# Kernel optimization log

Hardware: AMD Instinct MI355X
Metric: run time of the kernel (lower is better)

## Reference

```python
import jax, jax.numpy as jnp
import numpy as np

N_HEADS = 16

def setup_inputs() -> dict:
    key = jax.random.key(0)
    k1, k2, k3 = jax.random.split(key, 3)
    d = 1024
    x = jax.random.normal(k1, (4, 2048, d), dtype=jnp.float32)
    w_qkv = jax.random.normal(k2, (d, 3 * d), dtype=jnp.float32) * (1.0 / np.sqrt(d))
    w_proj = jax.random.normal(k3, (d, d), dtype=jnp.float32) * (1.0 / np.sqrt(d))
    return {"x": x, "w_qkv": w_qkv, "w_proj": w_proj}

def reference(x, w_qkv, w_proj):
    b, s, c = x.shape
    h = N_HEADS
    hd = c // h
    qkv = x @ w_qkv  # [b, s, 3c]
    q, k, v = jnp.split(qkv, 3, axis=-1)
    # [b, h, s, hd]
    q = q.reshape(b, s, h, hd).transpose(0, 2, 1, 3)
    k = k.reshape(b, s, h, hd).transpose(0, 2, 1, 3)
    v = v.reshape(b, s, h, hd).transpose(0, 2, 1, 3)
    scores = jnp.einsum('bhqd,bhkd->bhqk', q, k) / jnp.sqrt(jnp.float32(hd))
    causal = jnp.tril(jnp.ones((s, s), dtype=bool))
    scores = jnp.where(causal[None, None], scores, jnp.float32(-jnp.inf))
    attn = jax.nn.softmax(scores, axis=-1)
    out = jnp.einsum('bhqk,bhkd->bhqd', attn, v)
    out = out.transpose(0, 2, 1, 3).reshape(b, s, c)
    return out @ w_proj
```

## Files before the change

kernel.cpp:

```cpp
#include <hip/hip_runtime.h>
#include <hip/hip_bf16.h>

typedef unsigned short u16;
typedef __attribute__((ext_vector_type(8))) short short8;
typedef __attribute__((ext_vector_type(4))) float f32x4;
typedef __attribute__((ext_vector_type(16))) float f32x16;

__device__ inline u16 f2bf(float f) {
  unsigned u = __float_as_uint(f);
  u += 0x7fffu + ((u >> 16) & 1u);
  return (u16)(u >> 16);
}

__global__ __launch_bounds__(256) void cast_kernel(const float* __restrict__ in,
                                                   u16* __restrict__ out, int n4) {
  int i = blockIdx.x * 256 + threadIdx.x;
  if (i >= n4) return;
  float4 v = ((const float4*)in)[i];
  ushort4 o;
  o.x = f2bf(v.x); o.y = f2bf(v.y); o.z = f2bf(v.z); o.w = f2bf(v.w);
  ((ushort4*)out)[i] = o;
}

__global__ __launch_bounds__(256) void tcast_kernel(const float* __restrict__ in,
                                                    u16* __restrict__ out, int K, int N) {
  __shared__ float tile[32][33];
  int bx = blockIdx.x * 32;
  int by = blockIdx.y * 32;
  int tx = threadIdx.x & 31, ty = threadIdx.x >> 5;
#pragma unroll
  for (int i = 0; i < 4; i++) {
    int r = ty + i * 8;
    tile[r][tx] = in[(size_t)(by + r) * N + bx + tx];
  }
  __syncthreads();
#pragma unroll
  for (int i = 0; i < 4; i++) {
    int r = ty + i * 8;
    out[(size_t)(bx + r) * K + by + tx] = f2bf(tile[tx][r]);
  }
}

__global__ __launch_bounds__(256) void pack_kv(const u16* __restrict__ kbuf,
                                               const u16* __restrict__ vbuf,
                                               u16* __restrict__ kpack,
                                               u16* __restrict__ vpack) {
  __shared__ __align__(16) u16 ktile[64 * 72];
  __shared__ __align__(16) u16 vtile[64 * 72];
  int t = threadIdx.x;
  int kt = blockIdx.x, h = blockIdx.y, b = blockIdx.z;
  int bh = b * 16 + h;
  size_t rb = (size_t)(b * 2048 + kt * 64);
#pragma unroll
  for (int i = 0; i < 2; i++) {
    int idx = i * 256 + t; int r = idx >> 3, c8 = (idx & 7) * 8;
    *(uint4*)&ktile[r * 72 + c8] = *(const uint4*)(kbuf + (rb + r) * 1024 + h * 64 + c8);
    *(uint4*)&vtile[r * 72 + c8] = *(const uint4*)(vbuf + (rb + r) * 1024 + h * 64 + c8);
  }
  __syncthreads();
  u16* kd = kpack + ((size_t)bh * 32 + kt) * 4096;
  u16* vd = vpack + ((size_t)bh * 32 + kt) * 4096;
#pragma unroll
  for (int i = 0; i < 2; i++) {
    int idx = i * 256 + t;
    int j = idx >> 6, lane = idx & 63, l31 = lane & 31, hi5 = lane >> 5;
    *(uint4*)(kd + j * 512 + lane * 8) =
        *(const uint4*)&ktile[((j >> 2) * 32 + l31) * 72 + (j & 3) * 16 + hi5 * 8];
    union { u16 s[8]; uint4 u; } pv;
#pragma unroll
    for (int e = 0; e < 8; e++)
      pv.s[e] = vtile[((j & 3) * 16 + hi5 * 8 + e) * 72 + (j >> 2) * 32 + l31];
    *(uint4*)(vd + j * 512 + lane * 8) = pv.u;
  }
}

#define GEMM_BODY(KSTR)                                                                       \
  __shared__ __align__(16) u16 As[128 * 32];                                                  \
  __shared__ __align__(16) u16 Bs[128 * 32];                                                  \
  int t = threadIdx.x;                                                                        \
  int wave = t >> 6, lane = t & 63, l15 = lane & 15, quad = lane >> 4;                        \
  int bn = blockIdx.x * 128, bm = blockIdx.y * 128;                                           \
  int wm = (wave >> 1) * 64, wn = (wave & 1) * 64;                                            \
  f32x4 acc[4][4];                                                                            \
  for (int i = 0; i < 4; i++)                                                                 \
    for (int j = 0; j < 4; j++) acc[i][j] = (f32x4)0.0f;                                      \
  int srow = wave * 16 + (lane >> 2);                                                         \
  int scol = (lane & 3) * 8;                                                                  \
  const u16* ga0 = A + (size_t)(bm + srow) * KSTR + scol;                                     \
  const u16* ga1 = A + (size_t)(bm + 64 + srow) * KSTR + scol;                                \
  const u16* gb0 = Bt + (size_t)(bn + srow) * KSTR + scol;                                    \
  const u16* gb1 = Bt + (size_t)(bn + 64 + srow) * KSTR + scol;                               \
  u16* lA0 = As + wave * 512;                                                                 \
  u16* lA1 = As + 2048 + wave * 512;                                                          \
  u16* lB0 = Bs + wave * 512;                                                                 \
  u16* lB1 = Bs + 2048 + wave * 512;                                                          \
  for (int k0 = 0; k0 < KSTR; k0 += 32) {                                                     \
    __syncthreads();                                                                          \
    __builtin_amdgcn_global_load_lds((const __attribute__((address_space(1))) unsigned*)(ga0 + k0), \
                                     (__attribute__((address_space(3))) unsigned*)lA0, 16, 0, 0);   \
    __builtin_amdgcn_global_load_lds((const __attribute__((address_space(1))) unsigned*)(ga1 + k0), \
                                     (__attribute__((address_space(3))) unsigned*)lA1, 16, 0, 0);   \
    __builtin_amdgcn_global_load_lds((const __attribute__((address_space(1))) unsigned*)(gb0 + k0), \
                                     (__attribute__((address_space(3))) unsigned*)lB0, 16, 0, 0);   \
    __builtin_amdgcn_global_load_lds((const __attribute__((address_space(1))) unsigned*)(gb1 + k0), \
                                     (__attribute__((address_space(3))) unsigned*)lB1, 16, 0, 0);   \
    __syncthreads();                                                                          \
    short8 a[4], b[4];                                                                        \
    for (int mt = 0; mt < 4; mt++)                                                            \
      a[mt] = *(const short8*)(&As[(wm + mt * 16 + l15) * 32 + quad * 8]);                    \
    for (int nt = 0; nt < 4; nt++)                                                            \
      b[nt] = *(const short8*)(&Bs[(wn + nt * 16 + l15) * 32 + quad * 8]);                    \
    for (int mt = 0; mt < 4; mt++)                                                            \
      for (int nt = 0; nt < 4; nt++)                                                          \
        acc[mt][nt] = __builtin_amdgcn_mfma_f32_16x16x32_bf16(a[mt], b[nt], acc[mt][nt], 0, 0, 0); \
  }

__global__ __launch_bounds__(256) void gemm_qkv(const u16* __restrict__ A,
                                                const u16* __restrict__ Bt,
                                                u16* __restrict__ qb,
                                                u16* __restrict__ kb,
                                                u16* __restrict__ vb) {
  GEMM_BODY(1024)
  u16* dst = (bn < 1024) ? qb : (bn < 2048) ? kb : vb;
  float scl = (bn < 1024) ? 0.18033688011112f : 1.0f;
  int bnl = bn & 1023;
#pragma unroll
  for (int mt = 0; mt < 4; mt++)
#pragma unroll
    for (int nt = 0; nt < 4; nt++)
#pragma unroll
      for (int r = 0; r < 4; r++) {
        int row = bm + wm + mt * 16 + quad * 4 + r;
        int col = bnl + wn + nt * 16 + l15;
        dst[(size_t)row * 1024 + col] = f2bf(acc[mt][nt][r] * scl);
      }
}

__global__ __launch_bounds__(256) void gemm_proj(const u16* __restrict__ A,
                                                 const u16* __restrict__ Bt,
                                                 float* __restrict__ Co) {
  GEMM_BODY(1024)
#pragma unroll
  for (int mt = 0; mt < 4; mt++)
#pragma unroll
    for (int nt = 0; nt < 4; nt++)
#pragma unroll
      for (int r = 0; r < 4; r++) {
        int row = bm + wm + mt * 16 + quad * 4 + r;
        int col = bn + wn + nt * 16 + l15;
        Co[(size_t)row * 1024 + col] = acc[mt][nt][r];
      }
}

__global__ __launch_bounds__(256, 2) void attn_kernel(const u16* __restrict__ qbuf,
                                                      const u16* __restrict__ kpack,
                                                      const u16* __restrict__ vpack,
                                                      u16* __restrict__ ctx) {
  int t = threadIdx.x;
  int wave = t >> 6, lane = t & 63, l31 = lane & 31, hi = lane >> 5;
  int bh = blockIdx.x;
  int s = (int)blockIdx.y * 4 + wave;
  int b = bh >> 4, h = bh & 15;
  int rowbase = b * 2048;
  int hi4 = hi * 4;

  const u16* kp = kpack + (size_t)bh * (32 * 4096) + lane * 8;
  const u16* vp = vpack + (size_t)bh * (32 * 4096) + lane * 8;

#pragma unroll
  for (int ph = 0; ph < 2; ph++) {
    int strip = ph ? 63 - s : s;
    int q0 = strip * 32;
    int q_lane = q0 + l31;

    const u16* qp = qbuf + (size_t)(rowbase + q_lane) * 1024 + h * 64 + hi * 8;
    short8 qf[4];
#pragma unroll
    for (int ks = 0; ks < 4; ks++) qf[ks] = *(const short8*)(qp + ks * 16);

    float l_run = 0.0f;
    f32x16 o[2];
    o[0] = (f32x16)0.0f; o[1] = (f32x16)0.0f;
    int ktmax = (q0 + 31) >> 6;

    for (int kt = 0; kt <= ktmax; kt++) {
      const u16* kb = kp + kt * 4096;
      const u16* vb = vp + kt * 4096;

      short8 ka[8], vv[8];
#pragma unroll
      for (int j = 0; j < 8; j++) {
        ka[j] = *(const short8*)(kb + j * 512);
        vv[j] = *(const short8*)(vb + j * 512);
      }

      f32x16 st0 = (f32x16)0.0f, st1 = (f32x16)0.0f;
#pragma unroll
      for (int ks = 0; ks < 4; ks++) {
        st0 = __builtin_amdgcn_mfma_f32_32x32x16_bf16(ka[ks], qf[ks], st0, 0, 0, 0);
        st1 = __builtin_amdgcn_mfma_f32_32x32x16_bf16(ka[4 + ks], qf[ks], st1, 0, 0, 0);
      }

      unsigned pk[2][8];
      if (kt == ktmax) {
#pragma unroll
        for (int ii = 0; ii < 8; ii++) {
          int key = kt * 64 + ((2 * ii) & 3) + 8 * ((2 * ii) >> 2) + hi4;
          float p00 = (key     <= q_lane) ? __builtin_amdgcn_exp2f(st0[2 * ii])     : 0.0f;
          float p01 = (key + 1 <= q_lane) ? __builtin_amdgcn_exp2f(st0[2 * ii + 1]) : 0.0f;
          float p10 = (key + 32 <= q_lane) ? __builtin_amdgcn_exp2f(st1[2 * ii])     : 0.0f;
          float p11 = (key + 33 <= q_lane) ? __builtin_amdgcn_exp2f(st1[2 * ii + 1]) : 0.0f;
          l_run += p00 + p01 + p10 + p11;
          pk[0][ii] = ((__float_as_uint(p00) + 0x8000u) >> 16) |
                      ((__float_as_uint(p01) + 0x8000u) & 0xffff0000u);
          pk[1][ii] = ((__float_as_uint(p10) + 0x8000u) >> 16) |
                      ((__float_as_uint(p11) + 0x8000u) & 0xffff0000u);
        }
      } else {
#pragma unroll
        for (int ii = 0; ii < 8; ii++) {
          float p00 = __builtin_amdgcn_exp2f(st0[2 * ii]);
          float p01 = __builtin_amdgcn_exp2f(st0[2 * ii + 1]);
          float p10 = __builtin_amdgcn_exp2f(st1[2 * ii]);
          float p11 = __builtin_amdgcn_exp2f(st1[2 * ii + 1]);
          l_run += p00 + p01 + p10 + p11;
          pk[0][ii] = ((__float_as_uint(p00) + 0x8000u) >> 16) |
                      ((__float_as_uint(p01) + 0x8000u) & 0xffff0000u);
          pk[1][ii] = ((__float_as_uint(p10) + 0x8000u) >> 16) |
                      ((__float_as_uint(p11) + 0x8000u) & 0xffff0000u);
        }
      }

      short8 pf[4];
#pragma unroll
      for (int ks2 = 0; ks2 < 4; ks2++) {
        int km = ks2 >> 1, h4 = (ks2 & 1) * 4;
        unsigned A0 = pk[km][h4 + 0], A1 = pk[km][h4 + 1];
        unsigned B0 = pk[km][h4 + 2], B1 = pk[km][h4 + 3];
        unsigned tA0 = (unsigned)__shfl_xor((int)A0, 32);
        unsigned tA1 = (unsigned)__shfl_xor((int)A1, 32);
        unsigned tB0 = (unsigned)__shfl_xor((int)B0, 32);
        unsigned tB1 = (unsigned)__shfl_xor((int)B1, 32);
        union { unsigned u[4]; short8 sh; } fr;
        fr.u[0] = hi ? tB0 : A0;
        fr.u[1] = hi ? tB1 : A1;
        fr.u[2] = hi ? B0 : tA0;
        fr.u[3] = hi ? B1 : tA1;
        pf[ks2] = fr.sh;
      }

#pragma unroll
      for (int am = 0; am < 2; am++)
#pragma unroll
        for (int ks2 = 0; ks2 < 4; ks2++)
          o[am] = __builtin_amdgcn_mfma_f32_32x32x16_bf16(vv[am * 4 + ks2], pf[ks2], o[am], 0, 0, 0);
    }

    float l_tot = l_run + __shfl_xor(l_run, 32);
    float inv = 1.0f / l_tot;
    size_t obase = (size_t)(rowbase + q_lane) * 1024 + h * 64;
#pragma unroll
    for (int am = 0; am < 2; am++)
#pragma unroll
      for (int k = 0; k < 4; k++) {
        ushort4 w;
        w.x = f2bf(o[am][4 * k + 0] * inv);
        w.y = f2bf(o[am][4 * k + 1] * inv);
        w.z = f2bf(o[am][4 * k + 2] * inv);
        w.w = f2bf(o[am][4 * k + 3] * inv);
        *(ushort4*)&ctx[obase + am * 32 + k * 8 + hi4] = w;
      }
  }
}

extern "C" void kernel_launch(void* const* d_in, const int* in_sizes, int n_in,
                              void* d_out, int out_size, void* d_ws, size_t ws_size,
                              hipStream_t stream) {
  const float* x      = (const float*)d_in[0];
  const float* w_qkv  = (const float*)d_in[1];
  const float* w_proj = (const float*)d_in[2];
  float* out = (float*)d_out;

  char* ws = (char*)d_ws;
  const size_t MB = 1024 * 1024;
  u16* qbuf   = (u16*)(ws);
  u16* kbuf   = (u16*)(ws + 16 * MB);
  u16* vbuf   = (u16*)(ws + 32 * MB);
  u16* xb     = (u16*)(ws + 48 * MB);
  u16* kpack  = (u16*)(ws + 48 * MB);
  u16* vpack  = (u16*)(ws + 64 * MB);
  u16* wqkvT  = (u16*)(ws + 80 * MB);
  u16* wprojT = (u16*)(ws + 86 * MB);
  u16* ctx    = kbuf;

  cast_kernel<<<8192, 256, 0, stream>>>(x, xb, 2097152);
  tcast_kernel<<<dim3(96, 32), 256, 0, stream>>>(w_qkv, wqkvT, 1024, 3072);
  tcast_kernel<<<dim3(32, 32), 256, 0, stream>>>(w_proj, wprojT, 1024, 1024);

  gemm_qkv<<<dim3(24, 64), 256, 0, stream>>>(xb, wqkvT, qbuf, kbuf, vbuf);
  pack_kv<<<dim3(32, 16, 4), 256, 0, stream>>>(kbuf, vbuf, kpack, vpack);
  attn_kernel<<<dim3(64, 8), 256, 0, stream>>>(qbuf, kpack, vpack, ctx);
  gemm_proj<<<dim3(8, 64), 256, 0, stream>>>(ctx, wprojT, out);
}
```

Baseline: 256.8 us.

## Rewrite QKV GEMM with 256x256 tiles and 4-stage LDS pipeline

```diff
diff --git a/kernel.cpp b/kernel.cpp
--- a/kernel.cpp
+++ b/kernel.cpp
@@ -72,6 +72,150 @@
       pv.s[e] = vtile[((j & 3) * 16 + hi5 * 8 + e) * 72 + (j >> 2) * 32 + l31];
     *(uint4*)(vd + j * 512 + lane * 8) = pv.u;
   }
+}
+
+
+#define VMWAIT(n) asm volatile("s_waitcnt vmcnt(" #n ")" ::: "memory")
+#define LGKM0()                                              \
+  do {                                                       \
+    asm volatile("s_waitcnt lgkmcnt(0)" ::: "memory");       \
+    __builtin_amdgcn_sched_barrier(0);                       \
+  } while (0)
+#define BAR() asm volatile("s_barrier" ::: "memory")
+
+__device__ __forceinline__ void gll16(const u16* g, u16* l) {
+  __builtin_amdgcn_global_load_lds((const __attribute__((address_space(1))) unsigned*)g,
+                                   (__attribute__((address_space(3))) unsigned*)l, 16, 0, 0);
+}
+
+__global__ __launch_bounds__(512, 2) void gemm_qkv(const u16* __restrict__ A,
+                                                   const u16* __restrict__ Bt,
+                                                   u16* __restrict__ qb,
+                                                   u16* __restrict__ kb,
+                                                   u16* __restrict__ vb) {
+  __shared__ u16 lds[65536];
+  int tid = threadIdx.x;
+  int w = tid >> 6, lane = tid & 63, l15 = lane & 15, quad = lane >> 4;
+  int wr = w >> 2, wc = w & 3;
+
+  int bid = blockIdx.x;
+  int wgid = (bid & 7) * 48 + (bid >> 3);
+  int bm = (wgid / 12) * 256;
+  int bn3 = (wgid % 12) * 256;
+
+  int stc0 = w * 2, stc1 = w * 2 + 1;
+  int srow = lane >> 2;
+  int kswz = ((lane & 3) * 8) ^ ((lane >> 5) << 4);
+  const u16* gA0 = A + (size_t)(bm + stc0 * 16 + srow) * 1024 + kswz;
+  const u16* gA1 = A + (size_t)(bm + stc1 * 16 + srow) * 1024 + kswz;
+  const u16* gB0 = Bt + (size_t)(bn3 + stc0 * 16 + srow) * 1024 + kswz;
+  const u16* gB1 = Bt + (size_t)(bn3 + stc1 * 16 + srow) * 1024 + kswz;
+  int dA0 = stc0 * 512, dA1 = stc1 * 512;
+
+  int kq = (quad * 8) ^ ((l15 & 8) << 1);
+  int aoffB = wr * 4096 + l15 * 32 + kq;
+  int boffB = 8192 + wc * 2048 + l15 * 32 + kq;
+
+  f32x4 acc[8][4];
+#pragma unroll
+  for (int m = 0; m < 8; m++)
+#pragma unroll
+    for (int n = 0; n < 4; n++) acc[m][n] = (f32x4)0.0f;
+
+  short8 a0[4], a1[4], bb0[4], bb1[4];
+
+#define STAGE_A(t)                                     \
+  do {                                                 \
+    u16* s_ = lds + ((t) & 3) * 16384;                 \
+    gll16(gA0 + (t) * 32, s_ + dA0);                   \
+    gll16(gA1 + (t) * 32, s_ + dA1);                   \
+  } while (0)
+#define STAGE_B(t)                                     \
+  do {                                                 \
+    u16* s_ = lds + ((t) & 3) * 16384 + 8192;          \
+    gll16(gB0 + (t) * 32, s_ + dA0);                   \
+    gll16(gB1 + (t) * 32, s_ + dA1);                   \
+  } while (0)
+
+#define PHASE_A(t, bbcur, DOSTG, VMN)                                                          \
+  do {                                                                                         \
+    const u16* sl = lds + ((t) & 3) * 16384;                                                   \
+    _Pragma("unroll") for (int m = 0; m < 4; m++)                                              \
+        a1[m] = *(const short8*)(sl + aoffB + (m + 4) * 512);                                  \
+    if (DOSTG) STAGE_B((t) + 3);                                                               \
+    BAR();                                                                                     \
+    LGKM0();                                                                                   \
+    __builtin_amdgcn_s_setprio(1);                                                             \
+    _Pragma("unroll") for (int m = 0; m < 4; m++) _Pragma("unroll") for (int n = 0; n < 4; n++) \
+        acc[m][n] = __builtin_amdgcn_mfma_f32_16x16x32_bf16(a0[m], bbcur[n], acc[m][n], 0, 0, 0); \
+    __builtin_amdgcn_s_setprio(0);                                                             \
+    VMN;                                                                                       \
+    BAR();                                                                                     \
+  } while (0)
+
+#define PHASE_B(t, bbcur, bbnxt, DORD, DOSTG)                                                  \
+  do {                                                                                         \
+    if (DORD) {                                                                                \
+      const u16* sl = lds + (((t) + 1) & 3) * 16384;                                           \
+      _Pragma("unroll") for (int n = 0; n < 4; n++)                                            \
+          bbnxt[n] = *(const short8*)(sl + boffB + n * 512);                                   \
+      _Pragma("unroll") for (int m = 0; m < 4; m++)                                            \
+          a0[m] = *(const short8*)(sl + aoffB + m * 512);                                      \
+    }                                                                                          \
+    if (DOSTG) STAGE_A((t) + 4);                                                               \
+    BAR();                                                                                     \
+    LGKM0();                                                                                   \
+    __builtin_amdgcn_s_setprio(1);                                                             \
+    _Pragma("unroll") for (int m = 0; m < 4; m++) _Pragma("unroll") for (int n = 0; n < 4; n++) \
+        acc[m + 4][n] =                                                                        \
+            __builtin_amdgcn_mfma_f32_16x16x32_bf16(a1[m], bbcur[n], acc[m + 4][n], 0, 0, 0);  \
+    __builtin_amdgcn_s_setprio(0);                                                             \
+    BAR();                                                                                     \
+  } while (0)
+
+  STAGE_A(0); STAGE_B(0); STAGE_A(1); STAGE_B(1); STAGE_A(2); STAGE_B(2); STAGE_A(3);
+  VMWAIT(10);
+  BAR();
+  {
+    const u16* sl = lds;
+#pragma unroll
+    for (int n = 0; n < 4; n++) bb0[n] = *(const short8*)(sl + boffB + n * 512);
+#pragma unroll
+    for (int m = 0; m < 4; m++) a0[m] = *(const short8*)(sl + aoffB + m * 512);
+  }
+
+  for (int t = 0; t < 28; t += 2) {
+    PHASE_A(t, bb0, 1, VMWAIT(8));
+    PHASE_B(t, bb0, bb1, 1, 1);
+    PHASE_A(t + 1, bb1, 1, VMWAIT(8));
+    PHASE_B(t + 1, bb1, bb0, 1, 1);
+  }
+  PHASE_A(28, bb0, 1, VMWAIT(8));
+  PHASE_B(28, bb0, bb1, 1, 0);
+  PHASE_A(29, bb1, 0, VMWAIT(4));
+  PHASE_B(29, bb1, bb0, 1, 0);
+  PHASE_A(30, bb0, 0, VMWAIT(0));
+  PHASE_B(30, bb0, bb1, 1, 0);
+  PHASE_A(31, bb1, 0, );
+  PHASE_B(31, bb1, bb0, 0, 0);
+
+#undef PHASE_A
+#undef PHASE_B
+#undef STAGE_A
+#undef STAGE_B
+
+  u16* dst = (bn3 < 1024) ? qb : (bn3 < 2048) ? kb : vb;
+  float scl = (bn3 < 1024) ? 0.18033688011112f : 1.0f;
+  int bnl = bn3 & 1023;
+  int rbase = bm + wr * 128 + quad * 4;
+  int cbase = bnl + wc * 64 + l15;
+#pragma unroll
+  for (int m = 0; m < 8; m++)
+#pragma unroll
+    for (int n = 0; n < 4; n++)
+#pragma unroll
+      for (int r = 0; r < 4; r++)
+        dst[(size_t)(rbase + m * 16 + r) * 1024 + cbase + n * 16] = f2bf(acc[m][n][r] * scl);
 }
 
 #define GEMM_BODY(KSTR)                                                                       \
@@ -115,27 +259,6 @@
         acc[mt][nt] = __builtin_amdgcn_mfma_f32_16x16x32_bf16(a[mt], b[nt], acc[mt][nt], 0, 0, 0); \
   }
 
-__global__ __launch_bounds__(256) void gemm_qkv(const u16* __restrict__ A,
-                                                const u16* __restrict__ Bt,
-                                                u16* __restrict__ qb,
-                                                u16* __restrict__ kb,
-                                                u16* __restrict__ vb) {
-  GEMM_BODY(1024)
-  u16* dst = (bn < 1024) ? qb : (bn < 2048) ? kb : vb;
-  float scl = (bn < 1024) ? 0.18033688011112f : 1.0f;
-  int bnl = bn & 1023;
-#pragma unroll
-  for (int mt = 0; mt < 4; mt++)
-#pragma unroll
-    for (int nt = 0; nt < 4; nt++)
-#pragma unroll
-      for (int r = 0; r < 4; r++) {
-        int row = bm + wm + mt * 16 + quad * 4 + r;
-        int col = bnl + wn + nt * 16 + l15;
-        dst[(size_t)row * 1024 + col] = f2bf(acc[mt][nt][r] * scl);
-      }
-}
-
 __global__ __launch_bounds__(256) void gemm_proj(const u16* __restrict__ A,
                                                  const u16* __restrict__ Bt,
                                                  float* __restrict__ Co) {
@@ -297,7 +420,7 @@
   tcast_kernel<<<dim3(96, 32), 256, 0, stream>>>(w_qkv, wqkvT, 1024, 3072);
   tcast_kernel<<<dim3(32, 32), 256, 0, stream>>>(w_proj, wprojT, 1024, 1024);
 
-  gemm_qkv<<<dim3(24, 64), 256, 0, stream>>>(xb, wqkvT, qbuf, kbuf, vbuf);
+  gemm_qkv<<<dim3(384), 512, 0, stream>>>(xb, wqkvT, qbuf, kbuf, vbuf);
   pack_kv<<<dim3(32, 16, 4), 256, 0, stream>>>(kbuf, vbuf, kpack, vpack);
   attn_kernel<<<dim3(64, 8), 256, 0, stream>>>(qbuf, kpack, vpack, ctx);
   gemm_proj<<<dim3(8, 64), 256, 0, stream>>>(ctx, wprojT, out);
```

After: 258.2 us. Within noise of the previous version (+0.5%).
